# Kernel optimization log

Hardware: AMD Instinct MI355X
Metric: run time of the kernel (lower is better)

The kernel has to match this reference:

```python
import jax, jax.numpy as jnp
import numpy as np

HIDDEN = 4096
N_HEADS = 32
N_KV_HEADS = 8
HEAD_DIM = HIDDEN // N_HEADS  # 128
GROUPS = N_HEADS // N_KV_HEADS  # 4
B, S = 1, 2048
NEG = -1e9


def setup_inputs() -> dict:
    key = jax.random.key(0)
    ks = jax.random.split(key, 8)
    hidden_states = jax.random.normal(ks[0], (B, S, HIDDEN), dtype=jnp.float32)
    # additive causal mask [B,1,S,S]
    causal = jnp.tril(jnp.ones((S, S), dtype=bool))
    attention_mask = jnp.where(causal, 0.0, NEG).astype(jnp.float32)[None, None]
    position_ids = jnp.broadcast_to(jnp.arange(S, dtype=jnp.int64), (B, S))
    inv_freq = 1.0 / (500000.0 ** (np.arange(0, HEAD_DIM, 2, dtype=np.float32) / HEAD_DIM))
    freqs = np.arange(S, dtype=np.float32)[:, None] * inv_freq[None, :]  # [S, 64]
    cos = jnp.asarray(np.cos(freqs), dtype=jnp.float32)
    sin = jnp.asarray(np.sin(freqs), dtype=jnp.float32)
    sc = 1.0 / np.sqrt(HIDDEN)
    Wq = jax.random.normal(ks[1], (HIDDEN, HIDDEN), dtype=jnp.float32) * sc
    Wk = jax.random.normal(ks[2], (N_KV_HEADS * HEAD_DIM, HIDDEN), dtype=jnp.float32) * sc
    Wv = jax.random.normal(ks[3], (N_KV_HEADS * HEAD_DIM, HIDDEN), dtype=jnp.float32) * sc
    Wo = jax.random.normal(ks[4], (HIDDEN, HIDDEN), dtype=jnp.float32) * sc
    return {"hidden_states": hidden_states, "attention_mask": attention_mask,
            "position_ids": position_ids, "cos": cos, "sin": sin,
            "Wq": Wq, "Wk": Wk, "Wv": Wv, "Wo": Wo}


def _rope(q, k, cos, sin, position_ids):
    # cos/sin: [max_pos, head_dim//2]; gather per position -> [b,1,s,hd/2]
    c = cos[position_ids][:, None]  # [b,1,s,d/2]
    s_ = sin[position_ids][:, None]
    q1, q2 = q[..., ::2], q[..., 1::2]
    k1, k2 = k[..., ::2], k[..., 1::2]
    q_rot = jnp.concatenate([q1 * c - q2 * s_, q2 * c + q1 * s_], axis=-1)
    k_rot = jnp.concatenate([k1 * c - k2 * s_, k2 * c + k1 * s_], axis=-1)
    return q_rot, k_rot


def reference(hidden_states, attention_mask, position_ids, cos, sin, Wq, Wk, Wv, Wo):
    b, s, _ = hidden_states.shape
    q = jnp.einsum('bsh,oh->bso', hidden_states, Wq).reshape(b, s, N_HEADS, HEAD_DIM).transpose(0, 2, 1, 3)
    k = jnp.einsum('bsh,oh->bso', hidden_states, Wk).reshape(b, s, N_KV_HEADS, HEAD_DIM).transpose(0, 2, 1, 3)
    v = jnp.einsum('bsh,oh->bso', hidden_states, Wv).reshape(b, s, N_KV_HEADS, HEAD_DIM).transpose(0, 2, 1, 3)
    q, k = _rope(q, k, cos, sin, position_ids)
    if GROUPS > 1:
        k = jnp.repeat(k, GROUPS, axis=1)  # [b,H,s,d]
        v = jnp.repeat(v, GROUPS, axis=1)
    scores = jnp.einsum('bhqd,bhkd->bhqk', q, k) / np.sqrt(HEAD_DIM)
    scores = scores + attention_mask
    attn = jax.nn.softmax(scores.astype(jnp.float32), axis=-1).astype(q.dtype)
    out = jnp.einsum('bhqk,bhkd->bhqd', attn, v)
    out = out.transpose(0, 2, 1, 3).reshape(b, s, HIDDEN)
    out = jnp.einsum('bso,ho->bsh', out, Wo)
    return out
```

## Files before the change

kernel.cpp:

```cpp
#include <hip/hip_runtime.h>
#include <hip/hip_bf16.h>

#define S_LEN 2048
#define HID   4096
#define NH    32
#define NKV   8
#define HD    128

typedef __attribute__((ext_vector_type(8))) short short8v;
typedef __attribute__((ext_vector_type(4))) float floatx4;

__device__ __forceinline__ float bf2f(unsigned short u) {
  union { unsigned int u32; float f; } v; v.u32 = ((unsigned int)u) << 16; return v.f;
}
__device__ __forceinline__ unsigned short f2bf(float f) {
  union { float f; unsigned int u; } v; v.f = f;
  unsigned int u = v.u + 0x7fffu + ((v.u >> 16) & 1u);
  return (unsigned short)(u >> 16);
}
__device__ __forceinline__ unsigned int cvtpk_bf16(float lo, float hi) {
  unsigned int r;
  asm("v_cvt_pk_bf16_f32 %0, %1, %2" : "=v"(r) : "v"(lo), "v"(hi));
  return r;
}

__device__ __forceinline__ void gld_lds16(const void* g, void* l) {
  __builtin_amdgcn_global_load_lds((const __attribute__((address_space(1))) void*)g,
                                   (__attribute__((address_space(3))) void*)l, 16, 0, 0);
}

__global__ __launch_bounds__(256) void cvt_all(const float* __restrict__ X,  const float* __restrict__ Wq,
                                               const float* __restrict__ Wk, const float* __restrict__ Wv,
                                               const float* __restrict__ Wo,
                                               unsigned short* __restrict__ Xb,  unsigned short* __restrict__ Wqb,
                                               unsigned short* __restrict__ Wkb, unsigned short* __restrict__ Wvb,
                                               unsigned short* __restrict__ Wob) {
  const int c0 = 1048576;
  const int c1 = c0 + 2097152;
  const int c2 = c1 + 524288;
  const int c3 = c2 + 524288;
  const int c4 = c3 + 2097152;
  int i = blockIdx.x * blockDim.x + threadIdx.x;
  int stride = gridDim.x * blockDim.x;
  for (; i < c4; i += stride) {
    const float* src; unsigned short* dst; int off;
    if (i < c0)      { src = X;  dst = Xb;  off = i; }
    else if (i < c1) { src = Wq; dst = Wqb; off = i - c0; }
    else if (i < c2) { src = Wk; dst = Wkb; off = i - c1; }
    else if (i < c3) { src = Wv; dst = Wvb; off = i - c2; }
    else             { src = Wo; dst = Wob; off = i - c3; }
    float4 v0 = ((const float4*)src)[2 * off];
    float4 v1 = ((const float4*)src)[2 * off + 1];
    union { ushort4 h[2]; uint4 u; } o;
    o.h[0].x = f2bf(v0.x); o.h[0].y = f2bf(v0.y); o.h[0].z = f2bf(v0.z); o.h[0].w = f2bf(v0.w);
    o.h[1].x = f2bf(v1.x); o.h[1].y = f2bf(v1.y); o.h[1].z = f2bf(v1.z); o.h[1].w = f2bf(v1.w);
    ((uint4*)dst)[off] = o.u;
  }
}

__device__ __forceinline__ void gemm256_core(const unsigned short* __restrict__ A,
                                             const unsigned short* __restrict__ B,
                                             unsigned short* lds,
                                             int brow, int bcol, int tid,
                                             floatx4 acc[8][4]) {
  const int K = 4096;
  const int w = tid >> 6, lane = tid & 63;
  const int fr = lane & 15, fq = lane >> 4;
  const int wm = w >> 2, wn = w & 3;

  const int r0s = w * 32 + (lane >> 2);
  const int r1s = r0s + 16;
  const int sl0 = ((lane & 3) ^ ((r0s >> 1) & 3)) << 3;
  const int sl1 = ((lane & 3) ^ ((r1s >> 1) & 3)) << 3;
  const unsigned short* pAs0 = A + (size_t)(brow + r0s) * K + sl0;
  const unsigned short* pAs1 = A + (size_t)(brow + r1s) * K + sl1;
  const unsigned short* pBs0 = B + (size_t)(bcol + r0s) * K + sl0;
  const unsigned short* pBs1 = B + (size_t)(bcol + r1s) * K + sl1;

  const int sl = (fq ^ ((fr >> 1) & 3)) << 3;
  int aoffb[8], boffb[4];
#pragma unroll
  for (int m = 0; m < 8; ++m) aoffb[m] = (wm * 128 + m * 16 + fr) * 32 + sl;
#pragma unroll
  for (int n = 0; n < 4; ++n) boffb[n] = 16384 + (wn * 64 + n * 16 + fr) * 32 + sl;

#define STG_A(buf, kh, t)                                                     \
  do {                                                                        \
    const int ko_ = (t) * 64 + (kh) * 32;                                     \
    gld_lds16(pAs0 + ko_, lds + (buf) * 32768 + (kh) * 8192 + w * 1024);      \
    gld_lds16(pAs1 + ko_, lds + (buf) * 32768 + (kh) * 8192 + w * 1024 + 512);\
  } while (0)
#define STG_B(buf, kh, t)                                                     \
  do {                                                                        \
    const int ko_ = (t) * 64 + (kh) * 32;                                     \
    gld_lds16(pBs0 + ko_, lds + (buf) * 32768 + 16384 + (kh) * 8192 + w * 1024);      \
    gld_lds16(pBs1 + ko_, lds + (buf) * 32768 + 16384 + (kh) * 8192 + w * 1024 + 512);\
  } while (0)

  STG_A(0, 0, 0); STG_B(0, 0, 0);
  STG_A(0, 1, 0); STG_B(0, 1, 0);
  STG_A(1, 0, 1); STG_B(1, 0, 1);
  asm volatile("s_waitcnt vmcnt(8)" ::: "memory");
  __builtin_amdgcn_s_barrier();

  const int NT = K / 64;
  for (int t = 0; t < NT; ++t) {
    const int c = t & 1;
    const unsigned short* Lc = lds + c * 32768;
    short8v a_[8], b_[4];

#pragma unroll
    for (int m = 0; m < 8; ++m) a_[m] = *(const short8v*)&Lc[aoffb[m]];
#pragma unroll
    for (int n = 0; n < 4; ++n) b_[n] = *(const short8v*)&Lc[boffb[n]];
    if (t + 1 < NT) { STG_A(c ^ 1, 1, t + 1); STG_B(c ^ 1, 1, t + 1); }
    __builtin_amdgcn_s_setprio(1);
#pragma unroll
    for (int m = 0; m < 8; ++m)
#pragma unroll
      for (int n = 0; n < 4; ++n)
        acc[m][n] = __builtin_amdgcn_mfma_f32_16x16x32_bf16(a_[m], b_[n], acc[m][n], 0, 0, 0);
    __builtin_amdgcn_s_setprio(0);
    if (t == NT - 1) asm volatile("s_waitcnt vmcnt(0)" ::: "memory");
    else             asm volatile("s_waitcnt vmcnt(8)" ::: "memory");
    __builtin_amdgcn_s_barrier();

#pragma unroll
    for (int m = 0; m < 8; ++m) a_[m] = *(const short8v*)&Lc[8192 + aoffb[m]];
#pragma unroll
    for (int n = 0; n < 4; ++n) b_[n] = *(const short8v*)&Lc[8192 + boffb[n]];
    if (t + 2 < NT) { STG_A(c, 0, t + 2); STG_B(c, 0, t + 2); }
    __builtin_amdgcn_s_setprio(1);
#pragma unroll
    for (int m = 0; m < 8; ++m)
#pragma unroll
      for (int n = 0; n < 4; ++n)
        acc[m][n] = __builtin_amdgcn_mfma_f32_16x16x32_bf16(a_[m], b_[n], acc[m][n], 0, 0, 0);
    __builtin_amdgcn_s_setprio(0);
    if (t + 2 < NT)      asm volatile("s_waitcnt vmcnt(8)" ::: "memory");
    else if (t + 1 < NT) asm volatile("s_waitcnt vmcnt(4)" ::: "memory");
    else                 asm volatile("s_waitcnt vmcnt(0)" ::: "memory");
    __builtin_amdgcn_s_barrier();
  }
#undef STG_A
#undef STG_B
}

__global__ __launch_bounds__(512, 2) void gemm_qkv(const unsigned short* __restrict__ Xb,
                                                   const unsigned short* __restrict__ Wqb,
                                                   const unsigned short* __restrict__ Wkb,
                                                   const unsigned short* __restrict__ Wvb,
                                                   unsigned short* __restrict__ Qg,
                                                   unsigned short* __restrict__ Kg,
                                                   unsigned short* __restrict__ Vt) {
  __shared__ unsigned short lds[2 * 32768];
  const int bx = blockIdx.x;
  const unsigned short* B; unsigned short* C; int mode, bcol, ldc;
  if (bx < 16)      { B = Wqb; C = Qg; mode = 0; bcol = bx * 256;        ldc = HID;  }
  else if (bx < 20) { B = Wkb; C = Kg; mode = 0; bcol = (bx - 16) * 256; ldc = 1024; }
  else              { B = Wvb; C = Vt; mode = 1; bcol = (bx - 20) * 256; ldc = 0;    }
  const int brow = blockIdx.y * 256;
  const int tid = threadIdx.x;
  floatx4 acc[8][4] = {};
  gemm256_core(Xb, B, lds, brow, bcol, tid, acc);

  const int w = tid >> 6, lane = tid & 63;
  const int fr = lane & 15, fq = lane >> 4;
  const int wm = w >> 2, wn = w & 3;
  const int r0 = brow + wm * 128 + fq * 4;
  const int c0 = bcol + wn * 64 + fr;
  if (mode == 0) {
#pragma unroll
    for (int m = 0; m < 8; ++m)
#pragma unroll
      for (int n = 0; n < 4; ++n)
#pragma unroll
        for (int r = 0; r < 4; ++r)
          C[(size_t)(r0 + m * 16 + r) * ldc + c0 + n * 16] = f2bf(acc[m][n][r]);
  } else {
#pragma unroll
    for (int m = 0; m < 8; ++m)
#pragma unroll
      for (int n = 0; n < 4; ++n) {
        ushort4 pk;
        pk.x = f2bf(acc[m][n][0]); pk.y = f2bf(acc[m][n][1]);
        pk.z = f2bf(acc[m][n][2]); pk.w = f2bf(acc[m][n][3]);
        *(ushort4*)&Vt[(size_t)(c0 + n * 16) * S_LEN + (r0 + m * 16)] = pk;
      }
  }
}

__global__ __launch_bounds__(512, 2) void gemm_o(const unsigned short* __restrict__ Ao,
                                                 const unsigned short* __restrict__ Wob,
                                                 float* __restrict__ Out) {
  __shared__ unsigned short lds[2 * 24576];
  const int K = 4096;
  const int tid = threadIdx.x;
  const int w = tid >> 6, lane = tid & 63;
  const int fr = lane & 15, fq = lane >> 4;
  const int wm = w >> 1, wn = w & 1;
  const int brow = blockIdx.y * 256, bcol = blockIdx.x * 128;

  const int rA = tid >> 2;
  const int sA = ((tid & 3) ^ ((rA >> 1) & 3)) << 3;
  const unsigned short* pA0 = Ao  + (size_t)(brow + rA) * K + sA;
  const unsigned short* pA1 = Ao  + (size_t)(brow + 128 + rA) * K + sA;
  const unsigned short* pB0 = Wob + (size_t)(bcol + rA) * K + sA;

  const int sl = (fq ^ ((fr >> 1) & 3)) << 3;
  int aoff[4], boff[4];
#pragma unroll
  for (int m = 0; m < 4; ++m) aoff[m] = (wm * 64 + m * 16 + fr) * 32 + sl;
#pragma unroll
  for (int n = 0; n < 4; ++n) boff[n] = 16384 + (wn * 64 + n * 16 + fr) * 32 + sl;

  floatx4 acc[4][4] = {};

#define STG_KH(buf, kh, t)                                                       \
  do {                                                                           \
    const int ko_ = (t) * 64 + (kh) * 32;                                        \
    gld_lds16(pA0 + ko_, lds + (buf) * 24576 + (kh) * 8192 + w * 512);           \
    gld_lds16(pA1 + ko_, lds + (buf) * 24576 + (kh) * 8192 + 4096 + w * 512);    \
    gld_lds16(pB0 + ko_, lds + (buf) * 24576 + 16384 + (kh) * 4096 + w * 512);   \
  } while (0)

  STG_KH(0, 0, 0);
  STG_KH(0, 1, 0);
  STG_KH(1, 0, 1);
  asm volatile("s_waitcnt vmcnt(6)" ::: "memory");
  __builtin_amdgcn_s_barrier();

  const int NT = K / 64;
  for (int t = 0; t < NT; ++t) {
    const int c = t & 1;
    const unsigned short* Lc = lds + c * 24576;
    short8v a_[4], b_[4];

#pragma unroll
    for (int m = 0; m < 4; ++m) a_[m] = *(const short8v*)&Lc[aoff[m]];
#pragma unroll
    for (int n = 0; n < 4; ++n) b_[n] = *(const short8v*)&Lc[boff[n]];
    if (t + 1 < NT) STG_KH(c ^ 1, 1, t + 1);
    __builtin_amdgcn_s_setprio(1);
#pragma unroll
    for (int m = 0; m < 4; ++m)
#pragma unroll
      for (int n = 0; n < 4; ++n)
        acc[m][n] = __builtin_amdgcn_mfma_f32_16x16x32_bf16(a_[m], b_[n], acc[m][n], 0, 0, 0);
    __builtin_amdgcn_s_setprio(0);
    if (t + 1 < NT) asm volatile("s_waitcnt vmcnt(6)" ::: "memory");
    else            asm volatile("s_waitcnt vmcnt(0)" ::: "memory");
    __builtin_amdgcn_s_barrier();

#pragma unroll
    for (int m = 0; m < 4; ++m) a_[m] = *(const short8v*)&Lc[8192 + aoff[m]];
#pragma unroll
    for (int n = 0; n < 4; ++n) b_[n] = *(const short8v*)&Lc[4096 + boff[n]];
    if (t + 2 < NT) STG_KH(c, 0, t + 2);
    __builtin_amdgcn_s_setprio(1);
#pragma unroll
    for (int m = 0; m < 4; ++m)
#pragma unroll
      for (int n = 0; n < 4; ++n)
        acc[m][n] = __builtin_amdgcn_mfma_f32_16x16x32_bf16(a_[m], b_[n], acc[m][n], 0, 0, 0);
    __builtin_amdgcn_s_setprio(0);
    if (t + 2 < NT)      asm volatile("s_waitcnt vmcnt(6)" ::: "memory");
    else if (t + 1 < NT) asm volatile("s_waitcnt vmcnt(3)" ::: "memory");
    else                 asm volatile("s_waitcnt vmcnt(0)" ::: "memory");
    __builtin_amdgcn_s_barrier();
  }
#undef STG_KH

  const int r0 = brow + wm * 64 + fq * 4;
  const int c0 = bcol + wn * 64 + fr;
#pragma unroll
  for (int m = 0; m < 4; ++m)
#pragma unroll
    for (int n = 0; n < 4; ++n)
#pragma unroll
      for (int r = 0; r < 4; ++r)
        Out[(size_t)(r0 + m * 16 + r) * HID + c0 + n * 16] = acc[m][n][r];
}

__global__ __launch_bounds__(256) void rope_k(const unsigned short* __restrict__ In,
                                              const float* __restrict__ cosT,
                                              const float* __restrict__ sinT,
                                              unsigned short* __restrict__ Out) {
  int idx = blockIdx.x * 256 + threadIdx.x;
  int j = idx & 63;
  int s = (idx >> 6) & (S_LEN - 1);
  int h = idx >> 17;
  unsigned int pr = *(const unsigned int*)(In + (size_t)s * (NKV * HD) + h * HD + 2 * j);
  float k1 = bf2f((unsigned short)(pr & 0xffffu));
  float k2 = bf2f((unsigned short)(pr >> 16));
  float c = cosT[s * 64 + j], sn = sinT[s * 64 + j];
  unsigned int pk = (unsigned int)f2bf(k1 * c - k2 * sn) |
                    ((unsigned int)f2bf(k2 * c + k1 * sn) << 16);
  *(unsigned int*)(Out + ((size_t)h * S_LEN + s) * HD + 2 * j) = pk;
}

__global__ __launch_bounds__(512, 4) void attn_fwd(const unsigned short* __restrict__ Qg,
                                                   const float* __restrict__ cosT,
                                                   const float* __restrict__ sinT,
                                                   const unsigned short* __restrict__ Kr,
                                                   const unsigned short* __restrict__ Vt,
                                                   unsigned short* __restrict__ Ao) {
  __shared__ unsigned short Kl[2][64 * 128];
  __shared__ unsigned short Vl[2][128 * 64];
  const int id = blockIdx.x;
  const int xcd = id & 7, rr = id >> 3;
  const int qt = 15 - (rr >> 2);
  const int h  = xcd * 4 + (rr & 3);
  const int hk = h >> 2;
  const int qb = qt * 128;
  const int tid = threadIdx.x, w = tid >> 6, lane = tid & 63;
  const int fr = lane & 15, fq = lane >> 4;

  short8v aq[4];
  {
    const int s_row = qb + w * 16 + fr;
    const unsigned short* qp = Qg + (size_t)s_row * HID + h * HD + fq * 8;
    const float* cb = cosT + s_row * 64;
    const float* sb = sinT + s_row * 64;
    const float SC = 0.12751744f;
#pragma unroll
    for (int ks = 0; ks < 4; ++ks) {
      short8v raw = *(const short8v*)(qp + ks * 32);
      short8v ov;
#pragma unroll
      for (int e = 0; e < 4; ++e) {
        float q1 = bf2f((unsigned short)raw[2 * e]);
        float q2 = bf2f((unsigned short)raw[2 * e + 1]);
        int j = ks * 16 + fq * 4 + e;
        float c = cb[j], sn = sb[j];
        ov[2 * e]     = (short)f2bf(SC * (q1 * c - q2 * sn));
        ov[2 * e + 1] = (short)f2bf(SC * (q2 * c + q1 * sn));
      }
      aq[ks] = ov;
    }
  }

  const int kcb = ((tid & 15) * 16) ^ (((tid >> 4) & 7) << 4);
  const unsigned short* pK0 = Kr + ((size_t)hk * S_LEN + (tid >> 4)) * HD + (kcb >> 1);
  const int vcb = ((tid & 7) * 16) ^ (((tid >> 3) & 7) << 4);
  const unsigned short* pV0 = Vt + ((size_t)hk * HD + (tid >> 3)) * S_LEN + (vcb >> 1);

  const int hsel = fq >> 1;
  const int srcA = fr + ((2 * (fq & 1)) << 4);
  const int srcB = fr + ((2 * (fq & 1) + 1) << 4);

  float l_acc = 0.f;
  floatx4 o[8] = {};

#define STAGE(buf, t)                                                           \
  do {                                                                          \
    const unsigned short* pk_ = pK0 + (size_t)(t) * 64 * HD;                    \
    const unsigned short* pv_ = pV0 + (t) * 64;                                 \
    _Pragma("unroll")                                                           \
    for (int j = 0; j < 2; ++j)                                                 \
      gld_lds16(pk_ + (size_t)j * 32 * HD, &Kl[buf][j * 4096 + w * 512]);       \
    _Pragma("unroll")                                                           \
    for (int j = 0; j < 2; ++j)                                                 \
      gld_lds16(pv_ + (size_t)j * 64 * S_LEN, &Vl[buf][j * 4096 + w * 512]);    \
  } while (0)

  STAGE(0, 0);
  asm volatile("s_waitcnt vmcnt(0)" ::: "memory");
  __syncthreads();

  const int nt = 2 * qt + 2;
  int cur = 0;
  for (int t = 0; t < nt; ++t) {
    const int kv0 = t * 64;
    if (t + 1 < nt) STAGE(cur ^ 1, t + 1);

    floatx4 St[4] = {};
    const unsigned short* Kc = &Kl[cur][0];
    const unsigned short* Vc = &Vl[cur][0];
    __builtin_amdgcn_s_setprio(1);
#pragma unroll
    for (int ks = 0; ks < 4; ++ks) {
#pragma unroll
      for (int n = 0; n < 4; ++n) {
        int row = n * 16 + fr;
        int cb = (ks * 64 + fq * 16) ^ ((row & 7) << 4);
        short8v kf = *(const short8v*)&Kc[row * 128 + (cb >> 1)];
        St[n] = __builtin_amdgcn_mfma_f32_16x16x32_bf16(kf, aq[ks], St[n], 0, 0, 0);
      }
    }
    __builtin_amdgcn_s_setprio(0);

    if (t >= 2 * qt) {
#pragma unroll
      for (int n = 0; n < 4; ++n) {
#pragma unroll
        for (int r = 0; r < 4; ++r) {
          int kvg = kv0 + n * 16 + fq * 4 + r;
          if (kvg > qb + w * 16 + fr) St[n][r] = -1e30f;
        }
      }
    }

    unsigned int pk[4][2];
#pragma unroll
    for (int n = 0; n < 4; ++n) {
      float p0 = exp2f(St[n][0]);
      float p1 = exp2f(St[n][1]);
      float p2 = exp2f(St[n][2]);
      float p3 = exp2f(St[n][3]);
      l_acc += (p0 + p1) + (p2 + p3);
      pk[n][0] = cvtpk_bf16(p0, p1);
      pk[n][1] = cvtpk_bf16(p2, p3);
    }

    short8v pa[2];
#pragma unroll
    for (int ks = 0; ks < 2; ++ks) {
      unsigned int v0a = __shfl(pk[2 * ks][0], srcA), v0b = __shfl(pk[2 * ks + 1][0], srcA);
      unsigned int v1a = __shfl(pk[2 * ks][1], srcA), v1b = __shfl(pk[2 * ks + 1][1], srcA);
      unsigned int v2a = __shfl(pk[2 * ks][0], srcB), v2b = __shfl(pk[2 * ks + 1][0], srcB);
      unsigned int v3a = __shfl(pk[2 * ks][1], srcB), v3b = __shfl(pk[2 * ks + 1][1], srcB);
      uint4 u;
      u.x = hsel ? v0b : v0a;
      u.y = hsel ? v1b : v1a;
      u.z = hsel ? v2b : v2a;
      u.w = hsel ? v3b : v3a;
      pa[ks] = *(short8v*)&u;
    }

    __builtin_amdgcn_s_setprio(1);
#pragma unroll
    for (int nf = 0; nf < 8; ++nf) {
#pragma unroll
      for (int ks = 0; ks < 2; ++ks) {
        int row = nf * 16 + fr;
        int cb = (ks * 64 + fq * 16) ^ ((row & 7) << 4);
        short8v bv = *(const short8v*)&Vc[row * 64 + (cb >> 1)];
        o[nf] = __builtin_amdgcn_mfma_f32_16x16x32_bf16(pa[ks], bv, o[nf], 0, 0, 0);
      }
    }
    __builtin_amdgcn_s_setprio(0);

    if (t + 1 < nt) {
      asm volatile("s_waitcnt vmcnt(0)" ::: "memory");
      __syncthreads();
      cur ^= 1;
    }
  }
#undef STAGE

  float L = l_acc;
  L += __shfl_xor(L, 16);
  L += __shfl_xor(L, 32);
  float rinv[4];
#pragma unroll
  for (int r = 0; r < 4; ++r) rinv[r] = 1.0f / __shfl(L, fq * 4 + r);

  unsigned short* aop = Ao + (size_t)(qb + w * 16 + fq * 4) * HID + h * HD + fr;
#pragma unroll
  for (int nf = 0; nf < 8; ++nf)
#pragma unroll
    for (int r = 0; r < 4; ++r)
      aop[(size_t)r * HID + nf * 16] = f2bf(o[nf][r] * rinv[r]);
}

extern "C" void kernel_launch(void* const* d_in, const int* in_sizes, int n_in,
                              void* d_out, int out_size, void* d_ws, size_t ws_size,
                              hipStream_t stream) {
  (void)in_sizes; (void)n_in; (void)out_size; (void)ws_size;
  const float* X    = (const float*)d_in[0];
  const float* cosT = (const float*)d_in[3];
  const float* sinT = (const float*)d_in[4];
  const float* Wq   = (const float*)d_in[5];
  const float* Wk   = (const float*)d_in[6];
  const float* Wv   = (const float*)d_in[7];
  const float* Wo   = (const float*)d_in[8];

  char* ws = (char*)d_ws;
  size_t off = 0;
  auto alloc = [&](size_t bytes) { char* p = ws + off; off += (bytes + 255) & ~(size_t)255; return p; };
  unsigned short* Xb  = (unsigned short*)alloc((size_t)S_LEN * HID * 2);
  unsigned short* Wqb = (unsigned short*)alloc((size_t)HID * HID * 2);
  unsigned short* Wkb = (unsigned short*)alloc((size_t)1024 * HID * 2);
  unsigned short* Wvb = (unsigned short*)alloc((size_t)1024 * HID * 2);
  unsigned short* Wob = (unsigned short*)alloc((size_t)HID * HID * 2);
  unsigned short* Qg  = (unsigned short*)alloc((size_t)S_LEN * HID * 2);
  unsigned short* Kg  = (unsigned short*)alloc((size_t)S_LEN * 1024 * 2);
  unsigned short* Vt  = (unsigned short*)alloc((size_t)1024 * S_LEN * 2);
  unsigned short* Kr = Wqb;
  unsigned short* Ao = Xb;

  cvt_all<<<2048, 256, 0, stream>>>(X, Wq, Wk, Wv, Wo, Xb, Wqb, Wkb, Wvb, Wob);
  gemm_qkv<<<dim3(24, 8), 512, 0, stream>>>(Xb, Wqb, Wkb, Wvb, Qg, Kg, Vt);
  rope_k<<<(NKV * S_LEN * 64) / 256, 256, 0, stream>>>(Kg, cosT, sinT, Kr);
  attn_fwd<<<512, 512, 0, stream>>>(Qg, cosT, sinT, Kr, Vt, Ao);
  gemm_o<<<dim3(32, 8), 512, 0, stream>>>(Ao, Wob, (float*)d_out);
}
```

Baseline: 293.9 us.

## Retile fused QKV GEMM to 256x192 over concatenated weights to fill all CUs

The QKV projection kernel now treats Wq, Wk and Wv as one contiguous 6144-row weight matrix, relying on the three converted buffers being adjacent in the workspace. It uses 256x192 output tiles, so the grid grows from 24x8 to 32x8 blocks. The goal is to avoid leaving a quarter of the compute units idle on a 256-CU part. B-tile staging moves to a triple-buffered, full-K-step scheme with retuned vmcnt waits, and the epilogue routes each 16-column group to Q, K or transposed V. The trade-off is lower arithmetic intensity per tile and a dependence on the workspace layout keeping the weights contiguous.

```diff
diff --git a/kernel.cpp b/kernel.cpp
--- a/kernel.cpp
+++ b/kernel.cpp
@@ -58,136 +58,132 @@
   }
 }
 
-__device__ __forceinline__ void gemm256_core(const unsigned short* __restrict__ A,
-                                             const unsigned short* __restrict__ B,
-                                             unsigned short* lds,
-                                             int brow, int bcol, int tid,
-                                             floatx4 acc[8][4]) {
+__global__ __launch_bounds__(512, 2) void gemm_qkv(const unsigned short* __restrict__ Xb,
+                                                   const unsigned short* __restrict__ Bcat,
+                                                   unsigned short* __restrict__ Qg,
+                                                   unsigned short* __restrict__ Kg,
+                                                   unsigned short* __restrict__ Vt) {
+  __shared__ unsigned short lds[2 * 16384 + 3 * 12288];
   const int K = 4096;
+  const int tid = threadIdx.x;
   const int w = tid >> 6, lane = tid & 63;
   const int fr = lane & 15, fq = lane >> 4;
   const int wm = w >> 2, wn = w & 3;
+  const int brow = blockIdx.y * 256, bcol = blockIdx.x * 192;
 
   const int r0s = w * 32 + (lane >> 2);
   const int r1s = r0s + 16;
   const int sl0 = ((lane & 3) ^ ((r0s >> 1) & 3)) << 3;
   const int sl1 = ((lane & 3) ^ ((r1s >> 1) & 3)) << 3;
-  const unsigned short* pAs0 = A + (size_t)(brow + r0s) * K + sl0;
-  const unsigned short* pAs1 = A + (size_t)(brow + r1s) * K + sl1;
-  const unsigned short* pBs0 = B + (size_t)(bcol + r0s) * K + sl0;
-  const unsigned short* pBs1 = B + (size_t)(bcol + r1s) * K + sl1;
+  const unsigned short* pAs0 = Xb + (size_t)(brow + r0s) * K + sl0;
+  const unsigned short* pAs1 = Xb + (size_t)(brow + r1s) * K + sl1;
+
+  const unsigned short* pBs[3];
+#pragma unroll
+  for (int j = 0; j < 3; ++j) {
+    int c = tid + j * 512;
+    int khj = (c >= 768) ? 1 : 0;
+    int rowj = (c - khj * 768) >> 2;
+    int slotj = c & 3;
+    pBs[j] = Bcat + (size_t)(bcol + rowj) * K + khj * 32 +
+             ((slotj ^ ((rowj >> 1) & 3)) << 3);
+  }
 
   const int sl = (fq ^ ((fr >> 1) & 3)) << 3;
-  int aoffb[8], boffb[4];
+  int aoffb[8], boffb[3];
 #pragma unroll
   for (int m = 0; m < 8; ++m) aoffb[m] = (wm * 128 + m * 16 + fr) * 32 + sl;
 #pragma unroll
-  for (int n = 0; n < 4; ++n) boffb[n] = 16384 + (wn * 64 + n * 16 + fr) * 32 + sl;
+  for (int n = 0; n < 3; ++n) boffb[n] = (wn * 48 + n * 16 + fr) * 32 + sl;
 
 #define STG_A(buf, kh, t)                                                     \
   do {                                                                        \
     const int ko_ = (t) * 64 + (kh) * 32;                                     \
-    gld_lds16(pAs0 + ko_, lds + (buf) * 32768 + (kh) * 8192 + w * 1024);      \
-    gld_lds16(pAs1 + ko_, lds + (buf) * 32768 + (kh) * 8192 + w * 1024 + 512);\
+    gld_lds16(pAs0 + ko_, lds + (buf) * 16384 + (kh) * 8192 + w * 1024);      \
+    gld_lds16(pAs1 + ko_, lds + (buf) * 16384 + (kh) * 8192 + w * 1024 + 512);\
   } while (0)
-#define STG_B(buf, kh, t)                                                     \
+#define STG_B(bb, t)                                                          \
   do {                                                                        \
-    const int ko_ = (t) * 64 + (kh) * 32;                                     \
-    gld_lds16(pBs0 + ko_, lds + (buf) * 32768 + 16384 + (kh) * 8192 + w * 1024);      \
-    gld_lds16(pBs1 + ko_, lds + (buf) * 32768 + 16384 + (kh) * 8192 + w * 1024 + 512);\
+    const int ko_ = (t) * 64;                                                 \
+    gld_lds16(pBs[0] + ko_, lds + 32768 + (bb) * 12288 + w * 512);            \
+    gld_lds16(pBs[1] + ko_, lds + 32768 + (bb) * 12288 + 4096 + w * 512);     \
+    gld_lds16(pBs[2] + ko_, lds + 32768 + (bb) * 12288 + 8192 + w * 512);     \
   } while (0)
 
-  STG_A(0, 0, 0); STG_B(0, 0, 0);
-  STG_A(0, 1, 0); STG_B(0, 1, 0);
-  STG_A(1, 0, 1); STG_B(1, 0, 1);
-  asm volatile("s_waitcnt vmcnt(8)" ::: "memory");
+  floatx4 acc[8][3] = {};
+
+  STG_A(0, 0, 0); STG_A(0, 1, 0); STG_B(0, 0);
+  STG_A(1, 0, 1);                 STG_B(1, 1);
+  asm volatile("s_waitcnt vmcnt(5)" ::: "memory");
   __builtin_amdgcn_s_barrier();
 
   const int NT = K / 64;
   for (int t = 0; t < NT; ++t) {
     const int c = t & 1;
-    const unsigned short* Lc = lds + c * 32768;
-    short8v a_[8], b_[4];
-
-#pragma unroll
-    for (int m = 0; m < 8; ++m) a_[m] = *(const short8v*)&Lc[aoffb[m]];
-#pragma unroll
-    for (int n = 0; n < 4; ++n) b_[n] = *(const short8v*)&Lc[boffb[n]];
-    if (t + 1 < NT) { STG_A(c ^ 1, 1, t + 1); STG_B(c ^ 1, 1, t + 1); }
+    const int bb = t % 3;
+    const unsigned short* LA = lds + c * 16384;
+    const unsigned short* LB = lds + 32768 + bb * 12288;
+    short8v a_[8], b_[3];
+
+#pragma unroll
+    for (int m = 0; m < 8; ++m) a_[m] = *(const short8v*)&LA[aoffb[m]];
+#pragma unroll
+    for (int n = 0; n < 3; ++n) b_[n] = *(const short8v*)&LB[boffb[n]];
+    if (t + 1 < NT) STG_A(c ^ 1, 1, t + 1);
+    if (t + 2 < NT) STG_B((bb + 2) % 3, t + 2);
     __builtin_amdgcn_s_setprio(1);
 #pragma unroll
     for (int m = 0; m < 8; ++m)
 #pragma unroll
-      for (int n = 0; n < 4; ++n)
+      for (int n = 0; n < 3; ++n)
         acc[m][n] = __builtin_amdgcn_mfma_f32_16x16x32_bf16(a_[m], b_[n], acc[m][n], 0, 0, 0);
     __builtin_amdgcn_s_setprio(0);
-    if (t == NT - 1) asm volatile("s_waitcnt vmcnt(0)" ::: "memory");
-    else             asm volatile("s_waitcnt vmcnt(8)" ::: "memory");
-    __builtin_amdgcn_s_barrier();
-
-#pragma unroll
-    for (int m = 0; m < 8; ++m) a_[m] = *(const short8v*)&Lc[8192 + aoffb[m]];
-#pragma unroll
-    for (int n = 0; n < 4; ++n) b_[n] = *(const short8v*)&Lc[8192 + boffb[n]];
-    if (t + 2 < NT) { STG_A(c, 0, t + 2); STG_B(c, 0, t + 2); }
-    __builtin_amdgcn_s_setprio(1);
-#pragma unroll
-    for (int m = 0; m < 8; ++m)
-#pragma unroll
-      for (int n = 0; n < 4; ++n)
-        acc[m][n] = __builtin_amdgcn_mfma_f32_16x16x32_bf16(a_[m], b_[n], acc[m][n], 0, 0, 0);
-    __builtin_amdgcn_s_setprio(0);
-    if (t + 2 < NT)      asm volatile("s_waitcnt vmcnt(8)" ::: "memory");
-    else if (t + 1 < NT) asm volatile("s_waitcnt vmcnt(4)" ::: "memory");
+    if (t + 2 < NT)      asm volatile("s_waitcnt vmcnt(10)" ::: "memory");
+    else if (t + 1 < NT) asm volatile("s_waitcnt vmcnt(7)" ::: "memory");
     else                 asm volatile("s_waitcnt vmcnt(0)" ::: "memory");
     __builtin_amdgcn_s_barrier();
+
+#pragma unroll
+    for (int m = 0; m < 8; ++m) a_[m] = *(const short8v*)&LA[8192 + aoffb[m]];
+#pragma unroll
+    for (int n = 0; n < 3; ++n) b_[n] = *(const short8v*)&LB[6144 + boffb[n]];
+    if (t + 2 < NT) STG_A(c, 0, t + 2);
+    __builtin_amdgcn_s_setprio(1);
+#pragma unroll
+    for (int m = 0; m < 8; ++m)
+#pragma unroll
+      for (int n = 0; n < 3; ++n)
+        acc[m][n] = __builtin_amdgcn_mfma_f32_16x16x32_bf16(a_[m], b_[n], acc[m][n], 0, 0, 0);
+    __builtin_amdgcn_s_setprio(0);
+    if (t + 2 < NT)      asm volatile("s_waitcnt vmcnt(7)" ::: "memory");
+    else if (t + 1 < NT) asm volatile("s_waitcnt vmcnt(2)" ::: "memory");
+    else                 asm volatile("s_waitcnt vmcnt(0)" ::: "memory");
+    __builtin_amdgcn_s_barrier();
   }
 #undef STG_A
 #undef STG_B
-}
-
-__global__ __launch_bounds__(512, 2) void gemm_qkv(const unsigned short* __restrict__ Xb,
-                                                   const unsigned short* __restrict__ Wqb,
-                                                   const unsigned short* __restrict__ Wkb,
-                                                   const unsigned short* __restrict__ Wvb,
-                                                   unsigned short* __restrict__ Qg,
-                                                   unsigned short* __restrict__ Kg,
-                                                   unsigned short* __restrict__ Vt) {
-  __shared__ unsigned short lds[2 * 32768];
-  const int bx = blockIdx.x;
-  const unsigned short* B; unsigned short* C; int mode, bcol, ldc;
-  if (bx < 16)      { B = Wqb; C = Qg; mode = 0; bcol = bx * 256;        ldc = HID;  }
-  else if (bx < 20) { B = Wkb; C = Kg; mode = 0; bcol = (bx - 16) * 256; ldc = 1024; }
-  else              { B = Wvb; C = Vt; mode = 1; bcol = (bx - 20) * 256; ldc = 0;    }
-  const int brow = blockIdx.y * 256;
-  const int tid = threadIdx.x;
-  floatx4 acc[8][4] = {};
-  gemm256_core(Xb, B, lds, brow, bcol, tid, acc);
-
-  const int w = tid >> 6, lane = tid & 63;
-  const int fr = lane & 15, fq = lane >> 4;
-  const int wm = w >> 2, wn = w & 3;
+
   const int r0 = brow + wm * 128 + fq * 4;
-  const int c0 = bcol + wn * 64 + fr;
-  if (mode == 0) {
-#pragma unroll
-    for (int m = 0; m < 8; ++m)
-#pragma unroll
-      for (int n = 0; n < 4; ++n)
+#pragma unroll
+  for (int m = 0; m < 8; ++m)
+#pragma unroll
+    for (int n = 0; n < 3; ++n) {
+      const int bc = bcol + wn * 48 + n * 16;
+      if (bc < 4096) {
 #pragma unroll
         for (int r = 0; r < 4; ++r)
-          C[(size_t)(r0 + m * 16 + r) * ldc + c0 + n * 16] = f2bf(acc[m][n][r]);
-  } else {
-#pragma unroll
-    for (int m = 0; m < 8; ++m)
-#pragma unroll
-      for (int n = 0; n < 4; ++n) {
+          Qg[(size_t)(r0 + m * 16 + r) * HID + bc + fr] = f2bf(acc[m][n][r]);
+      } else if (bc < 5120) {
+#pragma unroll
+        for (int r = 0; r < 4; ++r)
+          Kg[(size_t)(r0 + m * 16 + r) * 1024 + bc - 4096 + fr] = f2bf(acc[m][n][r]);
+      } else {
         ushort4 pk;
         pk.x = f2bf(acc[m][n][0]); pk.y = f2bf(acc[m][n][1]);
         pk.z = f2bf(acc[m][n][2]); pk.w = f2bf(acc[m][n][3]);
-        *(ushort4*)&Vt[(size_t)(c0 + n * 16) * S_LEN + (r0 + m * 16)] = pk;
+        *(ushort4*)&Vt[(size_t)(bc - 5120 + fr) * S_LEN + (r0 + m * 16)] = pk;
       }
-  }
+    }
 }
 
 __global__ __launch_bounds__(512, 2) void gemm_o(const unsigned short* __restrict__ Ao,
@@ -491,7 +487,7 @@
   unsigned short* Ao = Xb;
 
   cvt_all<<<2048, 256, 0, stream>>>(X, Wq, Wk, Wv, Wo, Xb, Wqb, Wkb, Wvb, Wob);
-  gemm_qkv<<<dim3(24, 8), 512, 0, stream>>>(Xb, Wqb, Wkb, Wvb, Qg, Kg, Vt);
+  gemm_qkv<<<dim3(32, 8), 512, 0, stream>>>(Xb, Wqb, Qg, Kg, Vt);
   rope_k<<<(NKV * S_LEN * 64) / 256, 256, 0, stream>>>(Kg, cosT, sinT, Kr);
   attn_fwd<<<512, 512, 0, stream>>>(Qg, cosT, sinT, Kr, Vt, Ao);
   gemm_o<<<dim3(32, 8), 512, 0, stream>>>(Ao, Wob, (float*)d_out);
```

New measurement: 289.3 us, median of 2. Within noise of the previous version (-1.6%).
